# Performance work log

Hardware: AMD Instinct MI355X
Metric: run time of the kernel (lower is better)

The kernel has to match this reference:

```python
import jax, jax.numpy as jnp
import numpy as np

B = 256        # batch of LLR frames
N = 576        # code length (from wman_N0576_R34_z24)
MR = 144       # check rows = N * (1 - 3/4)
Z = 24         # lifting factor
IT = 3         # decoding iterations
ROW_DEG = 15   # check-node degree (WiMAX rate-3/4)


def setup_inputs() -> dict:
    key = jax.random.key(0)
    r = jax.random.normal(key, (B, N), dtype=jnp.float32)
    # Deterministic sparse Tanner graph: 15 ones per check row (>=2 required for top-2)
    rng = np.random.RandomState(0)
    Hnp = np.zeros((MR, N), dtype=np.int32)
    cols = np.argsort(rng.rand(MR, N), axis=1)[:, :ROW_DEG]
    Hnp[np.arange(MR)[:, None], cols] = 1
    H = jnp.asarray(Hnp)
    alpha = jnp.ones((MR // Z, N // Z, IT), dtype=jnp.float32) * 0.7
    beta = jnp.ones((MR // Z, N // Z, IT), dtype=jnp.float32) * 0.05
    return {"r": r, "alpha": alpha, "beta": beta, "H": H}


def _decode(r, alpha, beta, Hf):
    # r: (B, N) channel LLRs; Hf: (MR, N) float 0/1 parity-check mask
    mask = Hf == 1.0
    node = jnp.arange(N)[None, None, :]           # (1, 1, N)
    M = Hf[None, :, :] * r[:, None, :]            # initial v->c messages (B, MR, N)
    E = jnp.zeros_like(M)
    n_it = alpha.shape[-1]
    for it in range(n_it):
        a = jnp.repeat(jnp.repeat(alpha[:, :, it], Z, axis=0), Z, axis=1)  # (MR, N)
        bt = jnp.repeat(jnp.repeat(beta[:, :, it], Z, axis=0), Z, axis=1)  # (MR, N)
        # check -> variable: masked min-2 magnitude + extrinsic sign product
        abs_M = jnp.abs(M)
        masked = jnp.where(mask, abs_M, jnp.inf)
        neg_vals, idx = jax.lax.top_k(-masked, 2)  # two smallest per check row
        min_vals = -neg_vals                        # (B, MR, 2)
        # exclude self: use 2nd min at the argmin position, 1st min elsewhere
        E_abs = jnp.where(node == idx[..., 0:1], min_vals[..., 1:2], min_vals[..., 0:1])
        signs = jnp.where(mask, jnp.sign(M), 1.0)
        row_sign_prod = jnp.prod(signs, axis=2, keepdims=True)
        E_sign = row_sign_prod * signs              # extrinsic sign
        E = a * E_sign * jax.nn.relu(E_abs - bt) * Hf
        # variable -> check: sum-minus-self
        sum_E = jnp.sum(E, axis=1, keepdims=True)   # (B, 1, N)
        M = (r[:, None, :] + sum_E - E) * Hf
    return r + jnp.sum(E, axis=1)                   # posterior LLRs (B, N)


def reference(r, alpha, beta, H):
    return _decode(r, alpha, beta, H.astype(jnp.float32))
```

## Files before the change

kernel.cpp:

```cpp
#include <hip/hip_runtime.h>

#define BATCH   256
#define NCOL    576
#define MROW    144
#define ZLIFT   24
#define NIT     3
#define ROW_DEG 15
#define PKSTR   16
#define NSCIT   ((MROW/ZLIFT) * (NCOL/ZLIFT) * NIT)
#define TPB     512
#define CCAP    18
#define CSTR    19

__global__ __launch_bounds__(256) void build_cols_kernel(
    const int* __restrict__ H, int* __restrict__ pk)
{
    const int wave = (blockIdx.x * blockDim.x + threadIdx.x) >> 6;
    const int lane = threadIdx.x & 63;
    if (wave >= MROW) return;
    const int4* row4 = (const int4*)(H + (size_t)wave * NCOL);
    const int srow = (wave / ZLIFT) * (NCOL / ZLIFT);
    const unsigned long long below = (1ull << lane) - 1ull;
    int base = 0;
    #pragma unroll
    for (int r0 = 0; r0 < 3; ++r0) {
        const int vidx = r0 * 64 + lane;
        int4 h = make_int4(0, 0, 0, 0);
        if (vidx < NCOL / 4) h = row4[vidx];
        const int b0 = h.x != 0, b1 = h.y != 0, b2 = h.z != 0, b3 = h.w != 0;
        const unsigned long long m0 = __ballot(b0);
        const unsigned long long m1 = __ballot(b1);
        const unsigned long long m2 = __ballot(b2);
        const unsigned long long m3 = __ballot(b3);
        const int cnt_below = __popcll(m0 & below) + __popcll(m1 & below)
                            + __popcll(m2 & below) + __popcll(m3 & below);
        const int bits[4] = {b0, b1, b2, b3};
        const int n0 = vidx * 4;
        int pref = 0;
        #pragma unroll
        for (int c = 0; c < 4; ++c) {
            if (bits[c]) {
                const int idx = base + cnt_below + pref;
                const int n = n0 + c;
                if (idx < ROW_DEG)
                    pk[wave * PKSTR + idx] = n | ((srow + n / ZLIFT) << 16);
                ++pref;
            }
        }
        base += __popcll(m0) + __popcll(m1) + __popcll(m2) + __popcll(m3);
    }
}

__global__ __launch_bounds__(TPB) void ldpc_decode_kernel(
    const float* __restrict__ r,
    const float* __restrict__ alpha,
    const float* __restrict__ beta,
    const int*   __restrict__ pk,
    float*       __restrict__ out)
{
    __shared__ float r_s[NCOL];
    __shared__ float colsum[NCOL];
    __shared__ float E_s[NCOL * CSTR];
    __shared__ float a_s[NSCIT];
    __shared__ float b_s[NSCIT];
    __shared__ int   cdeg[NCOL];

    const int b   = blockIdx.x;
    const int tid = threadIdx.x;

    for (int n = tid; n < NCOL; n += TPB) {
        r_s[n]  = r[(size_t)b * NCOL + n];
        cdeg[n] = 0;
    }
    for (int i = tid; i < NCOL * CSTR; i += TPB) E_s[i] = 0.0f;
    if (tid < NSCIT) { a_s[tid] = alpha[tid]; b_s[tid] = beta[tid]; }
    __syncthreads();

    const bool is_row = (tid < MROW);
    int   pk_r[ROW_DEG];
    float r_r[ROW_DEG];
    float E_r[ROW_DEG];
    int   slot_r[ROW_DEG];
    if (is_row) {
        const int4* prow = (const int4*)(pk + tid * PKSTR);
        int4 q[4];
        #pragma unroll
        for (int j = 0; j < 4; ++j) q[j] = prow[j];
        const int* qi = (const int*)q;
        #pragma unroll
        for (int k = 0; k < ROW_DEG; ++k) {
            const int p = qi[k];
            pk_r[k] = p;
            const int n = p & 0xFFFF;
            r_r[k]  = r_s[n];
            E_r[k]  = 0.0f;
            slot_r[k] = n * CSTR + atomicAdd(&cdeg[n], 1);
        }
    }

    for (int it = 0; it < NIT; ++it) {
        if (is_row) {
            float vals[ROW_DEG];
            float min1 = INFINITY, min2 = INFINITY;
            int   kmin = -1;
            float sprod = 1.0f;
            #pragma unroll
            for (int k = 0; k < ROW_DEG; ++k) {
                float v;
                if (it == 0) {
                    v = r_r[k];
                } else {
                    const int n = pk_r[k] & 0xFFFF;
                    v = r_r[k] + colsum[n] - E_r[k];
                }
                vals[k] = v;
                const float av = fabsf(v);
                const float s = (v > 0.0f) ? 1.0f : ((v < 0.0f) ? -1.0f : 0.0f);
                sprod *= s;
                if (av < min1)      { min2 = min1; min1 = av; kmin = k; }
                else if (av < min2) { min2 = av; }
            }
            #pragma unroll
            for (int k = 0; k < ROW_DEG; ++k) {
                const int sidx = pk_r[k] >> 16;
                const float v = vals[k];
                const float s = (v > 0.0f) ? 1.0f : ((v < 0.0f) ? -1.0f : 0.0f);
                const float a  = a_s[sidx * NIT + it];
                const float bt = b_s[sidx * NIT + it];
                const float eabs = (k == kmin) ? min2 : min1;
                float mag = eabs - bt;
                if (mag < 0.0f) mag = 0.0f;
                const float E = a * (sprod * s) * mag;
                E_r[k] = E;
                E_s[slot_r[k]] = E;
            }
        }
        __syncthreads();

        if (it < NIT - 1) {
            for (int n = tid; n < NCOL; n += TPB) {
                const float* base = &E_s[n * CSTR];
                float sum = 0.0f;
                #pragma unroll
                for (int i = 0; i < CCAP; ++i) sum += base[i];
                colsum[n] = sum;
            }
            __syncthreads();
        } else {
            for (int n = tid; n < NCOL; n += TPB) {
                const float* base = &E_s[n * CSTR];
                float sum = 0.0f;
                #pragma unroll
                for (int i = 0; i < CCAP; ++i) sum += base[i];
                out[(size_t)b * NCOL + n] = r_s[n] + sum;
            }
        }
    }
}

extern "C" void kernel_launch(void* const* d_in, const int* in_sizes, int n_in,
                              void* d_out, int out_size, void* d_ws, size_t ws_size,
                              hipStream_t stream) {
    const float* r     = (const float*)d_in[0];
    const float* alpha = (const float*)d_in[1];
    const float* beta  = (const float*)d_in[2];
    const int*   H     = (const int*)d_in[3];
    float* out = (float*)d_out;
    int*   pk  = (int*)d_ws;

    build_cols_kernel<<<(MROW * 64 + 255) / 256, 256, 0, stream>>>(H, pk);
    ldpc_decode_kernel<<<BATCH, TPB, 0, stream>>>(r, alpha, beta, pk, out);
}
```

Before: 69.74 us.

## Split each check row across four lanes with shuffle-based min-2 reduction

Each check row is now handled by four threads, four edges each, instead of one thread serially walking all fifteen edges. Partial min1/min2/argmin/sign results are merged with xor shuffles. The block grows to 576 threads so every thread owns exactly one column for the column-sum and output phase. Alpha and beta are packed into a float2 table. This cuts per-row serial work and register pressure, and uses the whole block instead of only 144 active threads, at the cost of shuffle overhead and padding-lane masking.

```diff
diff --git a/kernel.cpp b/kernel.cpp
--- a/kernel.cpp
+++ b/kernel.cpp
@@ -8,7 +8,7 @@
 #define ROW_DEG 15
 #define PKSTR   16
 #define NSCIT   ((MROW/ZLIFT) * (NCOL/ZLIFT) * NIT)
-#define TPB     512
+#define TPB     576
 #define CCAP    18
 #define CSTR    19
 
@@ -21,6 +21,7 @@
     const int4* row4 = (const int4*)(H + (size_t)wave * NCOL);
     const int srow = (wave / ZLIFT) * (NCOL / ZLIFT);
     const unsigned long long below = (1ull << lane) - 1ull;
+    if (lane == 0) pk[wave * PKSTR + 15] = 0;
     int base = 0;
     #pragma unroll
     for (int r0 = 0; r0 < 3; ++r0) {
@@ -58,102 +59,106 @@
     const int*   __restrict__ pk,
     float*       __restrict__ out)
 {
-    __shared__ float r_s[NCOL];
-    __shared__ float colsum[NCOL];
-    __shared__ float E_s[NCOL * CSTR];
-    __shared__ float a_s[NSCIT];
-    __shared__ float b_s[NSCIT];
-    __shared__ int   cdeg[NCOL];
+    __shared__ float  r_s[NCOL];
+    __shared__ float  colsum[NCOL];
+    __shared__ float  E_s[NCOL * CSTR];
+    __shared__ float2 ab_s[NSCIT];
+    __shared__ int    cdeg[NCOL];
 
     const int b   = blockIdx.x;
     const int tid = threadIdx.x;
+    const int row = tid >> 2;
+    const int sub = tid & 3;
 
-    for (int n = tid; n < NCOL; n += TPB) {
-        r_s[n]  = r[(size_t)b * NCOL + n];
-        cdeg[n] = 0;
-    }
-    for (int i = tid; i < NCOL * CSTR; i += TPB) E_s[i] = 0.0f;
-    if (tid < NSCIT) { a_s[tid] = alpha[tid]; b_s[tid] = beta[tid]; }
+    r_s[tid]  = r[(size_t)b * NCOL + tid];
+    cdeg[tid] = 0;
+    #pragma unroll
+    for (int j = 0; j < CSTR; ++j) E_s[j * NCOL + tid] = 0.0f;
+    if (tid < NSCIT) ab_s[tid] = make_float2(alpha[tid], beta[tid]);
     __syncthreads();
 
-    const bool is_row = (tid < MROW);
-    int   pk_r[ROW_DEG];
-    float r_r[ROW_DEG];
-    float E_r[ROW_DEG];
-    int   slot_r[ROW_DEG];
-    if (is_row) {
-        const int4* prow = (const int4*)(pk + tid * PKSTR);
-        int4 q[4];
-        #pragma unroll
-        for (int j = 0; j < 4; ++j) q[j] = prow[j];
-        const int* qi = (const int*)q;
-        #pragma unroll
-        for (int k = 0; k < ROW_DEG; ++k) {
-            const int p = qi[k];
-            pk_r[k] = p;
-            const int n = p & 0xFFFF;
-            r_r[k]  = r_s[n];
-            E_r[k]  = 0.0f;
-            slot_r[k] = n * CSTR + atomicAdd(&cdeg[n], 1);
-        }
+    const int4 q = *(const int4*)(pk + row * PKSTR + sub * 4);
+    int pk_r[4] = {q.x, q.y, q.z, q.w};
+    float r_r[4], E_r[4];
+    int   slot_r[4];
+    #pragma unroll
+    for (int j = 0; j < 4; ++j) {
+        const int kglob = sub * 4 + j;
+        const int n = pk_r[j] & 0xFFFF;
+        r_r[j] = r_s[n];
+        E_r[j] = 0.0f;
+        if (kglob < ROW_DEG)
+            slot_r[j] = n * CSTR + atomicAdd(&cdeg[n], 1);
     }
 
     for (int it = 0; it < NIT; ++it) {
-        if (is_row) {
-            float vals[ROW_DEG];
-            float min1 = INFINITY, min2 = INFINITY;
-            int   kmin = -1;
-            float sprod = 1.0f;
-            #pragma unroll
-            for (int k = 0; k < ROW_DEG; ++k) {
-                float v;
-                if (it == 0) {
-                    v = r_r[k];
-                } else {
-                    const int n = pk_r[k] & 0xFFFF;
-                    v = r_r[k] + colsum[n] - E_r[k];
-                }
-                vals[k] = v;
-                const float av = fabsf(v);
+        float vals[4];
+        float min1 = INFINITY, min2 = INFINITY;
+        int   kmin = 1 << 30;
+        float sprod = 1.0f;
+        #pragma unroll
+        for (int j = 0; j < 4; ++j) {
+            const int kglob = sub * 4 + j;
+            const bool val = (kglob < ROW_DEG);
+            float v;
+            if (it == 0) {
+                v = r_r[j];
+            } else {
+                const int n = pk_r[j] & 0xFFFF;
+                v = r_r[j] + colsum[n] - E_r[j];
+            }
+            vals[j] = v;
+            const float av = val ? fabsf(v) : INFINITY;
+            const float s = val ? ((v > 0.0f) ? 1.0f : ((v < 0.0f) ? -1.0f : 0.0f))
+                                : 1.0f;
+            sprod *= s;
+            if (av < min1)      { min2 = min1; min1 = av; kmin = kglob; }
+            else if (av < min2) { min2 = av; }
+        }
+        #pragma unroll
+        for (int m = 1; m <= 2; m <<= 1) {
+            const float o1 = __shfl_xor(min1, m);
+            const float o2 = __shfl_xor(min2, m);
+            const int   ok = __shfl_xor(kmin, m);
+            const float os = __shfl_xor(sprod, m);
+            const bool self_lo = ((sub & m) == 0);
+            const float lo1 = self_lo ? min1 : o1;
+            const float lo2 = self_lo ? min2 : o2;
+            const int   lok = self_lo ? kmin : ok;
+            const float hi1 = self_lo ? o1 : min1;
+            const float hi2 = self_lo ? o2 : min2;
+            const int   hik = self_lo ? ok : kmin;
+            if (hi1 < lo1) { min1 = hi1; kmin = hik; min2 = fminf(hi2, lo1); }
+            else           { min1 = lo1; kmin = lok; min2 = fminf(lo2, hi1); }
+            sprod *= os;
+        }
+        #pragma unroll
+        for (int j = 0; j < 4; ++j) {
+            const int kglob = sub * 4 + j;
+            if (kglob < ROW_DEG) {
+                const int sidx = pk_r[j] >> 16;
+                const float v = vals[j];
                 const float s = (v > 0.0f) ? 1.0f : ((v < 0.0f) ? -1.0f : 0.0f);
-                sprod *= s;
-                if (av < min1)      { min2 = min1; min1 = av; kmin = k; }
-                else if (av < min2) { min2 = av; }
-            }
-            #pragma unroll
-            for (int k = 0; k < ROW_DEG; ++k) {
-                const int sidx = pk_r[k] >> 16;
-                const float v = vals[k];
-                const float s = (v > 0.0f) ? 1.0f : ((v < 0.0f) ? -1.0f : 0.0f);
-                const float a  = a_s[sidx * NIT + it];
-                const float bt = b_s[sidx * NIT + it];
-                const float eabs = (k == kmin) ? min2 : min1;
-                float mag = eabs - bt;
+                const float2 ab = ab_s[sidx * NIT + it];
+                const float eabs = (kglob == kmin) ? min2 : min1;
+                float mag = eabs - ab.y;
                 if (mag < 0.0f) mag = 0.0f;
-                const float E = a * (sprod * s) * mag;
-                E_r[k] = E;
-                E_s[slot_r[k]] = E;
+                const float E = ab.x * (sprod * s) * mag;
+                E_r[j] = E;
+                E_s[slot_r[j]] = E;
             }
         }
         __syncthreads();
 
+        const float* base = &E_s[tid * CSTR];
+        float sum = 0.0f;
+        #pragma unroll
+        for (int i = 0; i < CCAP; ++i) sum += base[i];
         if (it < NIT - 1) {
-            for (int n = tid; n < NCOL; n += TPB) {
-                const float* base = &E_s[n * CSTR];
-                float sum = 0.0f;
-                #pragma unroll
-                for (int i = 0; i < CCAP; ++i) sum += base[i];
-                colsum[n] = sum;
-            }
+            colsum[tid] = sum;
             __syncthreads();
         } else {
-            for (int n = tid; n < NCOL; n += TPB) {
-                const float* base = &E_s[n * CSTR];
-                float sum = 0.0f;
-                #pragma unroll
-                for (int i = 0; i < CCAP; ++i) sum += base[i];
-                out[(size_t)b * NCOL + n] = r_s[n] + sum;
-            }
+            out[(size_t)b * NCOL + tid] = r_s[tid] + sum;
         }
     }
 }
```

New measurement: 65.58 us. -6.0%, faster.
